# Performance work log

Hardware: AMD Instinct MI355X
Metric: run time of the kernel (lower is better)

Reference implementation:

```python
import jax, jax.numpy as jnp
import numpy as np

D = 1024      # in_dim
HS = 64       # head_size
H = 16        # num_heads
B, S = 2, 2048


def setup_inputs() -> dict:
    key = jax.random.key(0)
    k1, k2, k3, k4, k5, k6 = jax.random.split(key, 6)
    scale = 1.0 / np.sqrt(D)
    x = jax.random.normal(k1, (B, S, D), dtype=jnp.float32)
    # Stacked per-head projection weights (torch Linear weight is [out,in];
    # random init so layout only needs to be consistent). query weight exists
    # in the torch module but is never used (source bug), so it is omitted.
    Wk = jax.random.normal(k2, (H, D, HS), dtype=jnp.float32) * scale
    Wv = jax.random.normal(k3, (H, D, HS), dtype=jnp.float32) * scale
    Wproj = jax.random.normal(k4, (H * HS, D), dtype=jnp.float32) * (1.0 / np.sqrt(H * HS))
    bproj = jax.random.normal(k5, (D,), dtype=jnp.float32) * 0.01
    return {"x": x, "Wk": Wk, "Wv": Wv, "Wproj": Wproj, "bproj": bproj}


def reference(x, Wk, Wv, Wproj, bproj):
    # Faithful to source: k = key(x); q = value(x); v = value(x)  (q == v, no softmax)
    k = jnp.einsum("bsd,hde->bhse", x, Wk)   # [B,H,S,HS]
    v = jnp.einsum("bsd,hde->bhse", x, Wv)   # [B,H,S,HS]
    q = v
    inv_sqrt = jnp.asarray(HS, x.dtype) ** -0.5
    wei = jnp.einsum("bhse,bhte->bhst", q, k) * inv_sqrt  # [B,H,S,S], unnormalized
    out = jnp.einsum("bhst,bhte->bhse", wei, v)            # [B,H,S,HS]
    # concat heads: [B,S,H*HS]
    out = jnp.transpose(out, (0, 2, 1, 3)).reshape(x.shape[0], x.shape[1], H * HS)
    return out @ Wproj + bproj  # [B,S,D]
```

## Files before the change

kernel.cpp:

```cpp
#include <hip/hip_runtime.h>

#define B_ 2
#define S_ 2048
#define D_ 1024
#define H_ 16
#define HS_ 64
#define HD_ 1024
#define BS_ (B_*S_)
#define KS_ 64
#define TP_ 136

typedef __attribute__((ext_vector_type(8))) short short8_t;
typedef __attribute__((ext_vector_type(4))) float float4_t;

__device__ inline unsigned short f32_to_bf16(float f) {
  unsigned int u = __float_as_uint(f);
  u += 0x7FFF + ((u >> 16) & 1);
  return (unsigned short)(u >> 16);
}

__device__ inline void async_copy16(const void* g, void* lds) {
  __builtin_amdgcn_global_load_lds(
      (const __attribute__((address_space(1))) void*)g,
      (__attribute__((address_space(3))) void*)lds, 16, 0, 0);
}


__global__ __launch_bounds__(256) void prep_kernel(
    const float* __restrict__ x, const float* __restrict__ Wk,
    const float* __restrict__ Wv, unsigned short* __restrict__ xb,
    unsigned short* __restrict__ Wkvt) {
  const int blk = blockIdx.x;
  const int tid = threadIdx.x;
  __shared__ float lds[64][65];
  if (blk < 4096) {
    int idx = blk * 256 + tid;
    float4 v = ((const float4*)x)[idx];
    ushort4 o;
    o.x = f32_to_bf16(v.x); o.y = f32_to_bf16(v.y);
    o.z = f32_to_bf16(v.z); o.w = f32_to_bf16(v.w);
    ((ushort4*)xb)[idx] = o;
    return;
  }
  const int wblk = blk - 4096;
  const int h = wblk >> 4;
  const int d0 = (wblk & 15) * 64;
#pragma unroll
  for (int i = 0; i < 16; ++i) {
    int idx = tid + i * 256; int dd = idx >> 6, e = idx & 63;
    lds[e][dd] = Wk[((size_t)h * D_ + d0 + dd) * HS_ + e];
  }
  __syncthreads();
#pragma unroll
  for (int i = 0; i < 16; ++i) {
    int idx = tid + i * 256; int e = idx >> 6, dd = idx & 63;
    Wkvt[((size_t)h * 128 + e) * D_ + d0 + dd] = f32_to_bf16(lds[e][dd]);
  }
  __syncthreads();
#pragma unroll
  for (int i = 0; i < 16; ++i) {
    int idx = tid + i * 256; int dd = idx >> 6, e = idx & 63;
    lds[e][dd] = Wv[((size_t)h * D_ + d0 + dd) * HS_ + e];
  }
  __syncthreads();
#pragma unroll
  for (int i = 0; i < 16; ++i) {
    int idx = tid + i * 256; int e = idx >> 6, dd = idx & 63;
    Wkvt[((size_t)h * 128 + 64 + e) * D_ + d0 + dd] = f32_to_bf16(lds[e][dd]);
  }
}

__global__ __launch_bounds__(256) void kv_mfma_kernel(
    const unsigned short* __restrict__ xb,
    const unsigned short* __restrict__ Wkvt,
    unsigned short* __restrict__ Vb,
    float* __restrict__ Mpart) {
  const int blk = blockIdx.x;
  const int stile = blk & 31;
  const int h = blk >> 5;
  const int s0 = stile * 128;
  const int tid = threadIdx.x;
  const int lane = tid & 63;
  const int wid = tid >> 6;
  const int wm = wid & 1, wn = wid >> 1;
  const int quad = lane >> 4, l16 = lane & 15;
  const int srow8 = lane >> 3;
  const int sc8 = lane & 7;
  const int xa = l16 & 7;

  __shared__ __align__(16) unsigned char smem[65536];
  unsigned short* const A0 = (unsigned short*)smem;
  unsigned short* const B0 = (unsigned short*)(smem + 16384);
  unsigned short* const A1 = (unsigned short*)(smem + 32768);
  unsigned short* const B1 = (unsigned short*)(smem + 49152);
  unsigned short* Ktl = (unsigned short*)smem;
  unsigned short* Vtl = (unsigned short*)(smem + 64 * TP_ * 2);

  float4_t acc[4][4];
  const float4_t fz = {0.f, 0.f, 0.f, 0.f};
#pragma unroll
  for (int i = 0; i < 4; ++i)
#pragma unroll
    for (int j = 0; j < 4; ++j) acc[i][j] = fz;

  auto stage = [&](int kt, unsigned short* Ad, unsigned short* Bd) {
    const int k0 = kt * KS_;
#pragma unroll
    for (int i = 0; i < 4; ++i) {
      int g = wid * 4 + i;
      int r = g * 8 + srow8;
      int ch = (sc8 ^ (r & 7)) * 8;
      async_copy16(xb + (size_t)(s0 + r) * D_ + k0 + ch, Ad + g * 8 * KS_);
      async_copy16(Wkvt + ((size_t)h * 128 + r) * D_ + k0 + ch, Bd + g * 8 * KS_);
    }
  };
  auto compute = [&](const unsigned short* Ac, const unsigned short* Bc) {
#pragma unroll
    for (int ks = 0; ks < 2; ++ks) {
      short8_t a[4], b[4];
#pragma unroll
      for (int mi = 0; mi < 4; ++mi)
        a[mi] = *(const short8_t*)(Ac + (wm * 64 + mi * 16 + l16) * KS_ +
                                   ((ks * 4 + quad) ^ xa) * 8);
#pragma unroll
      for (int ni = 0; ni < 4; ++ni)
        b[ni] = *(const short8_t*)(Bc + (wn * 64 + ni * 16 + l16) * KS_ +
                                   ((ks * 4 + quad) ^ xa) * 8);
      __builtin_amdgcn_s_setprio(1);
#pragma unroll
      for (int mi = 0; mi < 4; ++mi)
#pragma unroll
        for (int ni = 0; ni < 4; ++ni)
          acc[mi][ni] = __builtin_amdgcn_mfma_f32_16x16x32_bf16(
              a[mi], b[ni], acc[mi][ni], 0, 0, 0);
      __builtin_amdgcn_s_setprio(0);
    }
  };

  stage(0, A0, B0);
#pragma unroll
  for (int t = 0; t < 16; ++t) {
    unsigned short* Ac = (t & 1) ? A1 : A0;
    unsigned short* Bc = (t & 1) ? B1 : B0;
    if (t < 15) {
      stage(t + 1, (t & 1) ? A0 : A1, (t & 1) ? B0 : B1);
      asm volatile("s_waitcnt vmcnt(8)" ::: "memory");
    } else {
      asm volatile("s_waitcnt vmcnt(0)" ::: "memory");
    }
    __builtin_amdgcn_s_barrier();
    __builtin_amdgcn_sched_barrier(0);
    compute(Ac, Bc);
    __builtin_amdgcn_sched_barrier(0);
    __builtin_amdgcn_s_barrier();
  }

  {
    unsigned short* dstT = (wn == 0) ? Ktl : Vtl;
#pragma unroll
    for (int mi = 0; mi < 4; ++mi)
#pragma unroll
      for (int ni = 0; ni < 4; ++ni) {
        int f = ni * 16 + l16;
        int sm = wm * 64 + mi * 16 + quad * 4;
        ushort4 o;
        o.x = f32_to_bf16(acc[mi][ni][0]);
        o.y = f32_to_bf16(acc[mi][ni][1]);
        o.z = f32_to_bf16(acc[mi][ni][2]);
        o.w = f32_to_bf16(acc[mi][ni][3]);
        *(ushort4*)&dstT[f * TP_ + sm] = o;
      }
  }
  __syncthreads();

#pragma unroll
  for (int u = 0; u < 4; ++u) {
    int unit = tid + u * 256;
    int s = unit & 127;
    int ec = (unit >> 7) * 8;
    union { unsigned short u16[8]; uint4 v; } t;
#pragma unroll
    for (int e = 0; e < 8; ++e) t.u16[e] = Vtl[(ec + e) * TP_ + s];
    *(uint4*)&Vb[(size_t)(s0 + s) * HD_ + h * 64 + ec] = t.v;
  }

  {
    float4_t macc[4];
#pragma unroll
    for (int ni = 0; ni < 4; ++ni) macc[ni] = fz;
#pragma unroll
    for (int ss = 0; ss < 4; ++ss) {
      short8_t ka = *(const short8_t*)&Ktl[(wid * 16 + l16) * TP_ + ss * 32 + quad * 8];
#pragma unroll
      for (int ni = 0; ni < 4; ++ni) {
        short8_t vv = *(const short8_t*)&Vtl[(ni * 16 + l16) * TP_ + ss * 32 + quad * 8];
        macc[ni] = __builtin_amdgcn_mfma_f32_16x16x32_bf16(ka, vv, macc[ni], 0, 0, 0);
      }
    }
    float* mdst = Mpart + ((size_t)stile * H_ + h) * 4096;
#pragma unroll
    for (int ni = 0; ni < 4; ++ni) {
      int e = ni * 16 + l16;
#pragma unroll
      for (int r = 0; r < 4; ++r) {
        int f = wid * 16 + quad * 4 + r;
        mdst[f * 64 + e] = macc[ni][r];
      }
    }
  }
}

__global__ __launch_bounds__(256) void m_reduce_kernel(
    const float* __restrict__ Mpart, float* __restrict__ M) {
  const int gid = blockIdx.x * 256 + threadIdx.x;
  const int e0 = gid * 4;
  const int bh = e0 >> 12;
  const int idx = e0 & 4095;
  const int b = bh >> 4, h = bh & 15;
  float4 s = {0.f, 0.f, 0.f, 0.f};
#pragma unroll
  for (int p = 0; p < 16; ++p) {
    const float4 v =
        *(const float4*)&Mpart[(((size_t)(b * 16 + p)) * H_ + h) * 4096 + idx];
    s.x += v.x; s.y += v.y; s.z += v.z; s.w += v.w;
  }
  s.x *= 0.125f; s.y *= 0.125f; s.z *= 0.125f; s.w *= 0.125f;
  *(float4*)&M[(size_t)bh * 4096 + idx] = s;
}

__global__ __launch_bounds__(256) void p_kernel(
    const float* __restrict__ M, const float* __restrict__ Wproj,
    unsigned short* __restrict__ Pt) {
  const int blk = blockIdx.x;
  const int dtile = blk & 15;
  const int h = (blk >> 4) & 15;
  const int b = blk >> 8;
  const int d0 = dtile * 64;
  const int tid = threadIdx.x;
  const int tx = tid & 15, ty = tid >> 4;
  __shared__ float Ms[64][68];
  __shared__ float Ws[64][68];
  const size_t mbase = ((size_t)(b * H_ + h)) * HS_ * HS_;
#pragma unroll
  for (int i = 0; i < 16; ++i) {
    int idx = tid + i * 256;
    int f = idx >> 6, e = idx & 63;
    Ms[e][f] = M[mbase + idx];
    Ws[f][e] = Wproj[(size_t)(h * HS_ + f) * D_ + d0 + e];
  }
  __syncthreads();
  float acc[4][4] = {};
#pragma unroll
  for (int kk = 0; kk < 64; ++kk) {
    const float4 a4 = *(const float4*)&Ms[kk][ty * 4];
    const float4 b4 = *(const float4*)&Ws[kk][tx * 4];
    const float a[4] = {a4.x, a4.y, a4.z, a4.w};
    const float bb[4] = {b4.x, b4.y, b4.z, b4.w};
#pragma unroll
    for (int i = 0; i < 4; ++i)
#pragma unroll
      for (int j = 0; j < 4; ++j) acc[i][j] += a[i] * bb[j];
  }
  __syncthreads();
#pragma unroll
  for (int i = 0; i < 4; ++i)
#pragma unroll
    for (int j = 0; j < 4; ++j)
      Ms[tx * 4 + j][ty * 4 + i] = acc[i][j];
  __syncthreads();
  {
    int c = tid >> 2, ch = tid & 3;
    unsigned short* dst = Pt + ((size_t)(b * D_ + d0 + c)) * HD_ + h * 64 + ch * 16;
#pragma unroll
    for (int e = 0; e < 16; ++e) dst[e] = f32_to_bf16(Ms[c][ch * 16 + e]);
  }
}

__global__ __launch_bounds__(256) void out_mfma_kernel(
    const unsigned short* __restrict__ Vb,
    const unsigned short* __restrict__ Pt,
    const float* __restrict__ bproj,
    float* __restrict__ out) {
  const int blk = blockIdx.x;
  const int ntile = blk & 15;
  const int stile = blk >> 4;
  const int s0 = stile * 128;
  const int n0 = ntile * 64;
  const int b = s0 >> 11;
  const int tid = threadIdx.x;
  const int lane = tid & 63;
  const int wid = tid >> 6;
  const int wm = wid & 1, wn = wid >> 1;
  const int quad = lane >> 4, l16 = lane & 15;
  const int srow8 = lane >> 3;
  const int sc8 = lane & 7;
  const int xa = l16 & 7;

  __shared__ __align__(16) unsigned char smem[49152];
  unsigned short* const A0 = (unsigned short*)smem;
  unsigned short* const B0 = (unsigned short*)(smem + 16384);
  unsigned short* const A1 = (unsigned short*)(smem + 24576);
  unsigned short* const B1 = (unsigned short*)(smem + 40960);

  float4_t acc[4][2];
  const float4_t fz = {0.f, 0.f, 0.f, 0.f};
#pragma unroll
  for (int i = 0; i < 4; ++i)
#pragma unroll
    for (int j = 0; j < 2; ++j) acc[i][j] = fz;

  const unsigned short* Bpanel = Pt + (size_t)b * D_ * HD_;
  auto stage = [&](int kt, unsigned short* Ad, unsigned short* Bd) {
    const int k0 = kt * KS_;
#pragma unroll
    for (int i = 0; i < 4; ++i) {
      int g = wid * 4 + i;
      int r = g * 8 + srow8;
      int ch = (sc8 ^ (r & 7)) * 8;
      async_copy16(Vb + (size_t)(s0 + r) * HD_ + k0 + ch, Ad + g * 8 * KS_);
    }
#pragma unroll
    for (int i = 0; i < 2; ++i) {
      int g = wid * 2 + i;
      int r = g * 8 + srow8;
      int ch = (sc8 ^ (r & 7)) * 8;
      async_copy16(Bpanel + (size_t)(n0 + r) * HD_ + k0 + ch, Bd + g * 8 * KS_);
    }
  };
  auto compute = [&](const unsigned short* Ac, const unsigned short* Bc) {
#pragma unroll
    for (int ks = 0; ks < 2; ++ks) {
      short8_t a[4], bfr[2];
#pragma unroll
      for (int mi = 0; mi < 4; ++mi)
        a[mi] = *(const short8_t*)(Ac + (wm * 64 + mi * 16 + l16) * KS_ +
                                   ((ks * 4 + quad) ^ xa) * 8);
#pragma unroll
      for (int ni = 0; ni < 2; ++ni)
        bfr[ni] = *(const short8_t*)(Bc + (wn * 32 + ni * 16 + l16) * KS_ +
                                     ((ks * 4 + quad) ^ xa) * 8);
      __builtin_amdgcn_s_setprio(1);
#pragma unroll
      for (int mi = 0; mi < 4; ++mi)
#pragma unroll
        for (int ni = 0; ni < 2; ++ni)
          acc[mi][ni] = __builtin_amdgcn_mfma_f32_16x16x32_bf16(
              a[mi], bfr[ni], acc[mi][ni], 0, 0, 0);
      __builtin_amdgcn_s_setprio(0);
    }
  };

  stage(0, A0, B0);
#pragma unroll
  for (int t = 0; t < 16; ++t) {
    unsigned short* Ac = (t & 1) ? A1 : A0;
    unsigned short* Bc = (t & 1) ? B1 : B0;
    if (t < 15) {
      stage(t + 1, (t & 1) ? A0 : A1, (t & 1) ? B0 : B1);
      asm volatile("s_waitcnt vmcnt(6)" ::: "memory");
    } else {
      asm volatile("s_waitcnt vmcnt(0)" ::: "memory");
    }
    __builtin_amdgcn_s_barrier();
    __builtin_amdgcn_sched_barrier(0);
    compute(Ac, Bc);
    __builtin_amdgcn_sched_barrier(0);
    __builtin_amdgcn_s_barrier();
  }

#pragma unroll
  for (int ni = 0; ni < 2; ++ni) {
    int col = n0 + wn * 32 + ni * 16 + l16;
    float bias = bproj[col];
#pragma unroll
    for (int mi = 0; mi < 4; ++mi) {
      int rowb = s0 + wm * 64 + mi * 16 + quad * 4;
#pragma unroll
      for (int r = 0; r < 4; ++r)
        out[(size_t)(rowb + r) * D_ + col] = acc[mi][ni][r] + bias;
    }
  }
}

extern "C" void kernel_launch(void* const* d_in, const int* in_sizes, int n_in,
                              void* d_out, int out_size, void* d_ws, size_t ws_size,
                              hipStream_t stream) {
  const float* x = (const float*)d_in[0];
  const float* Wk = (const float*)d_in[1];
  const float* Wv = (const float*)d_in[2];
  const float* Wproj = (const float*)d_in[3];
  const float* bproj = (const float*)d_in[4];
  float* out = (float*)d_out;

  char* ws = (char*)d_ws;
  unsigned short* xb = (unsigned short*)ws;
  unsigned short* Wkvt = xb + (size_t)BS_ * D_;
  unsigned short* Vb = Wkvt + (size_t)H_ * 128 * D_;
  float* Mpart = (float*)(Vb + (size_t)BS_ * HD_);
  float* M = Mpart + (size_t)32 * H_ * 4096;
  unsigned short* Pt = (unsigned short*)(M + (size_t)B_ * H_ * 4096);

  prep_kernel<<<dim3(4096 + H_ * (D_ / 64)), dim3(256), 0, stream>>>(x, Wk, Wv, xb, Wkvt);
  kv_mfma_kernel<<<dim3(32 * H_), dim3(256), 0, stream>>>(xb, Wkvt, Vb, Mpart);
  m_reduce_kernel<<<dim3(128), dim3(256), 0, stream>>>(Mpart, M);
  p_kernel<<<dim3(B_ * H_ * (D_ / 64)), dim3(256), 0, stream>>>(M, Wproj, Pt);
  out_mfma_kernel<<<dim3(32 * 16), dim3(256), 0, stream>>>(Vb, Pt, bproj, out);
}
```

Baseline: 128.4 us.

## Double block tiles to 512 threads and split K-step loads into two phases

The KV projection kernel now covers 256 sequence rows per block with 8 waves, and the output GEMM covers 128 columns per block, so each weight/P tile loaded into LDS is reused across more rows. Each K-step's staging is split in two halves, with the second half issued between the two MFMA sub-phases so loads are spread across the compute. The M partial products are still written per 128-row half, so the reduce layout is unchanged. This trades fewer blocks (256 vs 512) and larger LDS footprint for better reuse, at the risk of lower occupancy and extra barriers per iteration.

```diff
diff --git a/kernel.cpp b/kernel.cpp
--- a/kernel.cpp
+++ b/kernel.cpp
@@ -8,7 +8,7 @@
 #define HD_ 1024
 #define BS_ (B_*S_)
 #define KS_ 64
-#define TP_ 136
+#define TP2_ 264
 
 typedef __attribute__((ext_vector_type(8))) short short8_t;
 typedef __attribute__((ext_vector_type(4))) float float4_t;
@@ -70,31 +70,31 @@
   }
 }
 
-__global__ __launch_bounds__(256) void kv_mfma_kernel(
+__global__ __launch_bounds__(512) void kv_mfma_kernel(
     const unsigned short* __restrict__ xb,
     const unsigned short* __restrict__ Wkvt,
     unsigned short* __restrict__ Vb,
     float* __restrict__ Mpart) {
   const int blk = blockIdx.x;
-  const int stile = blk & 31;
-  const int h = blk >> 5;
-  const int s0 = stile * 128;
+  const int stile = blk & 15;
+  const int h = blk >> 4;
+  const int s0 = stile * 256;
   const int tid = threadIdx.x;
   const int lane = tid & 63;
   const int wid = tid >> 6;
-  const int wm = wid & 1, wn = wid >> 1;
+  const int wm = wid >> 1, wn = wid & 1;
   const int quad = lane >> 4, l16 = lane & 15;
   const int srow8 = lane >> 3;
   const int sc8 = lane & 7;
   const int xa = l16 & 7;
 
-  __shared__ __align__(16) unsigned char smem[65536];
+  __shared__ __align__(16) unsigned char smem[98304];
   unsigned short* const A0 = (unsigned short*)smem;
-  unsigned short* const B0 = (unsigned short*)(smem + 16384);
-  unsigned short* const A1 = (unsigned short*)(smem + 32768);
-  unsigned short* const B1 = (unsigned short*)(smem + 49152);
-  unsigned short* Ktl = (unsigned short*)smem;
-  unsigned short* Vtl = (unsigned short*)(smem + 64 * TP_ * 2);
+  unsigned short* const B0 = (unsigned short*)(smem + 32768);
+  unsigned short* const A1 = (unsigned short*)(smem + 49152);
+  unsigned short* const B1 = (unsigned short*)(smem + 81920);
+  unsigned short* const Ktl = (unsigned short*)smem;
+  unsigned short* const Vtl = (unsigned short*)(smem + 64 * TP2_ * 2);
 
   float4_t acc[4][4];
   const float4_t fz = {0.f, 0.f, 0.f, 0.f};
@@ -103,54 +103,65 @@
 #pragma unroll
     for (int j = 0; j < 4; ++j) acc[i][j] = fz;
 
-  auto stage = [&](int kt, unsigned short* Ad, unsigned short* Bd) {
+  auto stage_half = [&](int kt, unsigned short* Ad, unsigned short* Bd, int hf) {
     const int k0 = kt * KS_;
 #pragma unroll
-    for (int i = 0; i < 4; ++i) {
-      int g = wid * 4 + i;
+    for (int i = 0; i < 2; ++i) {
+      int g = wid * 4 + hf * 2 + i;
       int r = g * 8 + srow8;
       int ch = (sc8 ^ (r & 7)) * 8;
       async_copy16(xb + (size_t)(s0 + r) * D_ + k0 + ch, Ad + g * 8 * KS_);
+    }
+    {
+      int g = wid * 2 + hf;
+      int r = g * 8 + srow8;
+      int ch = (sc8 ^ (r & 7)) * 8;
       async_copy16(Wkvt + ((size_t)h * 128 + r) * D_ + k0 + ch, Bd + g * 8 * KS_);
     }
   };
-  auto compute = [&](const unsigned short* Ac, const unsigned short* Bc) {
-#pragma unroll
-    for (int ks = 0; ks < 2; ++ks) {
-      short8_t a[4], b[4];
-#pragma unroll
-      for (int mi = 0; mi < 4; ++mi)
-        a[mi] = *(const short8_t*)(Ac + (wm * 64 + mi * 16 + l16) * KS_ +
-                                   ((ks * 4 + quad) ^ xa) * 8);
+  auto compute_phase = [&](const unsigned short* Ac, const unsigned short* Bc,
+                           int ks) {
+    short8_t a[4], b[4];
+#pragma unroll
+    for (int mi = 0; mi < 4; ++mi)
+      a[mi] = *(const short8_t*)(Ac + (wm * 64 + mi * 16 + l16) * KS_ +
+                                 ((ks * 4 + quad) ^ xa) * 8);
+#pragma unroll
+    for (int ni = 0; ni < 4; ++ni)
+      b[ni] = *(const short8_t*)(Bc + (wn * 64 + ni * 16 + l16) * KS_ +
+                                 ((ks * 4 + quad) ^ xa) * 8);
+    __builtin_amdgcn_s_setprio(1);
+#pragma unroll
+    for (int mi = 0; mi < 4; ++mi)
 #pragma unroll
       for (int ni = 0; ni < 4; ++ni)
-        b[ni] = *(const short8_t*)(Bc + (wn * 64 + ni * 16 + l16) * KS_ +
-                                   ((ks * 4 + quad) ^ xa) * 8);
-      __builtin_amdgcn_s_setprio(1);
-#pragma unroll
-      for (int mi = 0; mi < 4; ++mi)
-#pragma unroll
-        for (int ni = 0; ni < 4; ++ni)
-          acc[mi][ni] = __builtin_amdgcn_mfma_f32_16x16x32_bf16(
-              a[mi], b[ni], acc[mi][ni], 0, 0, 0);
-      __builtin_amdgcn_s_setprio(0);
-    }
+        acc[mi][ni] = __builtin_amdgcn_mfma_f32_16x16x32_bf16(
+            a[mi], b[ni], acc[mi][ni], 0, 0, 0);
+    __builtin_amdgcn_s_setprio(0);
   };
 
-  stage(0, A0, B0);
-#pragma unroll
+  stage_half(0, A0, B0, 0);
+  stage_half(0, A0, B0, 1);
   for (int t = 0; t < 16; ++t) {
     unsigned short* Ac = (t & 1) ? A1 : A0;
     unsigned short* Bc = (t & 1) ? B1 : B0;
+    unsigned short* An = (t & 1) ? A0 : A1;
+    unsigned short* Bn = (t & 1) ? B0 : B1;
     if (t < 15) {
-      stage(t + 1, (t & 1) ? A0 : A1, (t & 1) ? B0 : B1);
-      asm volatile("s_waitcnt vmcnt(8)" ::: "memory");
+      stage_half(t + 1, An, Bn, 0);
+      asm volatile("s_waitcnt vmcnt(3)" ::: "memory");
     } else {
       asm volatile("s_waitcnt vmcnt(0)" ::: "memory");
     }
     __builtin_amdgcn_s_barrier();
     __builtin_amdgcn_sched_barrier(0);
-    compute(Ac, Bc);
+    compute_phase(Ac, Bc, 0);
+    __builtin_amdgcn_sched_barrier(0);
+    __builtin_amdgcn_s_barrier();
+    if (t < 15) stage_half(t + 1, An, Bn, 1);
+    __builtin_amdgcn_s_barrier();
+    __builtin_amdgcn_sched_barrier(0);
+    compute_phase(Ac, Bc, 1);
     __builtin_amdgcn_sched_barrier(0);
     __builtin_amdgcn_s_barrier();
   }
@@ -168,42 +179,45 @@
         o.y = f32_to_bf16(acc[mi][ni][1]);
         o.z = f32_to_bf16(acc[mi][ni][2]);
         o.w = f32_to_bf16(acc[mi][ni][3]);
-        *(ushort4*)&dstT[f * TP_ + sm] = o;
+        *(ushort4*)&dstT[f * TP2_ + sm] = o;
       }
   }
   __syncthreads();
 
 #pragma unroll
   for (int u = 0; u < 4; ++u) {
-    int unit = tid + u * 256;
-    int s = unit & 127;
-    int ec = (unit >> 7) * 8;
-    union { unsigned short u16[8]; uint4 v; } t;
-#pragma unroll
-    for (int e = 0; e < 8; ++e) t.u16[e] = Vtl[(ec + e) * TP_ + s];
-    *(uint4*)&Vb[(size_t)(s0 + s) * HD_ + h * 64 + ec] = t.v;
+    int unit = tid + u * 512;
+    int s = unit & 255;
+    int ec = (unit >> 8) * 8;
+    union { unsigned short u16[8]; uint4 v; } tv;
+#pragma unroll
+    for (int e = 0; e < 8; ++e) tv.u16[e] = Vtl[(ec + e) * TP2_ + s];
+    *(uint4*)&Vb[(size_t)(s0 + s) * HD_ + h * 64 + ec] = tv.v;
   }
 
   {
+    const int half = wid >> 2, fq = wid & 3;
     float4_t macc[4];
 #pragma unroll
     for (int ni = 0; ni < 4; ++ni) macc[ni] = fz;
 #pragma unroll
     for (int ss = 0; ss < 4; ++ss) {
-      short8_t ka = *(const short8_t*)&Ktl[(wid * 16 + l16) * TP_ + ss * 32 + quad * 8];
+      short8_t ka = *(const short8_t*)&Ktl[(fq * 16 + l16) * TP2_ +
+                                           half * 128 + ss * 32 + quad * 8];
 #pragma unroll
       for (int ni = 0; ni < 4; ++ni) {
-        short8_t vv = *(const short8_t*)&Vtl[(ni * 16 + l16) * TP_ + ss * 32 + quad * 8];
+        short8_t vv = *(const short8_t*)&Vtl[(ni * 16 + l16) * TP2_ +
+                                             half * 128 + ss * 32 + quad * 8];
         macc[ni] = __builtin_amdgcn_mfma_f32_16x16x32_bf16(ka, vv, macc[ni], 0, 0, 0);
       }
     }
-    float* mdst = Mpart + ((size_t)stile * H_ + h) * 4096;
+    float* mdst = Mpart + (((size_t)(stile * 2 + half)) * H_ + h) * 4096;
 #pragma unroll
     for (int ni = 0; ni < 4; ++ni) {
       int e = ni * 16 + l16;
 #pragma unroll
       for (int r = 0; r < 4; ++r) {
-        int f = wid * 16 + quad * 4 + r;
+        int f = fq * 16 + quad * 4 + r;
         mdst[f * 64 + e] = macc[ni][r];
       }
     }
@@ -276,16 +290,16 @@
   }
 }
 
-__global__ __launch_bounds__(256) void out_mfma_kernel(
+__global__ __launch_bounds__(512) void out_mfma_kernel(
     const unsigned short* __restrict__ Vb,
     const unsigned short* __restrict__ Pt,
     const float* __restrict__ bproj,
     float* __restrict__ out) {
   const int blk = blockIdx.x;
-  const int ntile = blk & 15;
-  const int stile = blk >> 4;
+  const int ntile = blk & 7;
+  const int stile = blk >> 3;
   const int s0 = stile * 128;
-  const int n0 = ntile * 64;
+  const int n0 = ntile * 128;
   const int b = s0 >> 11;
   const int tid = threadIdx.x;
   const int lane = tid & 63;
@@ -296,11 +310,11 @@
   const int sc8 = lane & 7;
   const int xa = l16 & 7;
 
-  __shared__ __align__(16) unsigned char smem[49152];
+  __shared__ __align__(16) unsigned char smem[65536];
   unsigned short* const A0 = (unsigned short*)smem;
   unsigned short* const B0 = (unsigned short*)(smem + 16384);
-  unsigned short* const A1 = (unsigned short*)(smem + 24576);
-  unsigned short* const B1 = (unsigned short*)(smem + 40960);
+  unsigned short* const A1 = (unsigned short*)(smem + 32768);
+  unsigned short* const B1 = (unsigned short*)(smem + 49152);
 
   float4_t acc[4][2];
   const float4_t fz = {0.f, 0.f, 0.f, 0.f};
@@ -310,60 +324,64 @@
     for (int j = 0; j < 2; ++j) acc[i][j] = fz;
 
   const unsigned short* Bpanel = Pt + (size_t)b * D_ * HD_;
-  auto stage = [&](int kt, unsigned short* Ad, unsigned short* Bd) {
+  auto stage_half = [&](int kt, unsigned short* Ad, unsigned short* Bd, int hf) {
     const int k0 = kt * KS_;
-#pragma unroll
-    for (int i = 0; i < 4; ++i) {
-      int g = wid * 4 + i;
+    {
+      int g = wid * 2 + hf;
       int r = g * 8 + srow8;
       int ch = (sc8 ^ (r & 7)) * 8;
       async_copy16(Vb + (size_t)(s0 + r) * HD_ + k0 + ch, Ad + g * 8 * KS_);
     }
-#pragma unroll
-    for (int i = 0; i < 2; ++i) {
-      int g = wid * 2 + i;
+    {
+      int g = wid * 2 + hf;
       int r = g * 8 + srow8;
       int ch = (sc8 ^ (r & 7)) * 8;
       async_copy16(Bpanel + (size_t)(n0 + r) * HD_ + k0 + ch, Bd + g * 8 * KS_);
     }
   };
-  auto compute = [&](const unsigned short* Ac, const unsigned short* Bc) {
-#pragma unroll
-    for (int ks = 0; ks < 2; ++ks) {
-      short8_t a[4], bfr[2];
-#pragma unroll
-      for (int mi = 0; mi < 4; ++mi)
-        a[mi] = *(const short8_t*)(Ac + (wm * 64 + mi * 16 + l16) * KS_ +
+  auto compute_phase = [&](const unsigned short* Ac, const unsigned short* Bc,
+                           int ks) {
+    short8_t a[4], bfr[2];
+#pragma unroll
+    for (int mi = 0; mi < 4; ++mi)
+      a[mi] = *(const short8_t*)(Ac + (wm * 64 + mi * 16 + l16) * KS_ +
+                                 ((ks * 4 + quad) ^ xa) * 8);
+#pragma unroll
+    for (int ni = 0; ni < 2; ++ni)
+      bfr[ni] = *(const short8_t*)(Bc + (wn * 32 + ni * 16 + l16) * KS_ +
                                    ((ks * 4 + quad) ^ xa) * 8);
+    __builtin_amdgcn_s_setprio(1);
+#pragma unroll
+    for (int mi = 0; mi < 4; ++mi)
 #pragma unroll
       for (int ni = 0; ni < 2; ++ni)
-        bfr[ni] = *(const short8_t*)(Bc + (wn * 32 + ni * 16 + l16) * KS_ +
-                                     ((ks * 4 + quad) ^ xa) * 8);
-      __builtin_amdgcn_s_setprio(1);
-#pragma unroll
-      for (int mi = 0; mi < 4; ++mi)
-#pragma unroll
-        for (int ni = 0; ni < 2; ++ni)
-          acc[mi][ni] = __builtin_amdgcn_mfma_f32_16x16x32_bf16(
-              a[mi], bfr[ni], acc[mi][ni], 0, 0, 0);
-      __builtin_amdgcn_s_setprio(0);
-    }
+        acc[mi][ni] = __builtin_amdgcn_mfma_f32_16x16x32_bf16(
+            a[mi], bfr[ni], acc[mi][ni], 0, 0, 0);
+    __builtin_amdgcn_s_setprio(0);
   };
 
-  stage(0, A0, B0);
-#pragma unroll
+  stage_half(0, A0, B0, 0);
+  stage_half(0, A0, B0, 1);
   for (int t = 0; t < 16; ++t) {
     unsigned short* Ac = (t & 1) ? A1 : A0;
     unsigned short* Bc = (t & 1) ? B1 : B0;
+    unsigned short* An = (t & 1) ? A0 : A1;
+    unsigned short* Bn = (t & 1) ? B0 : B1;
     if (t < 15) {
-      stage(t + 1, (t & 1) ? A0 : A1, (t & 1) ? B0 : B1);
-      asm volatile("s_waitcnt vmcnt(6)" ::: "memory");
+      stage_half(t + 1, An, Bn, 0);
+      asm volatile("s_waitcnt vmcnt(2)" ::: "memory");
     } else {
       asm volatile("s_waitcnt vmcnt(0)" ::: "memory");
     }
     __builtin_amdgcn_s_barrier();
     __builtin_amdgcn_sched_barrier(0);
-    compute(Ac, Bc);
+    compute_phase(Ac, Bc, 0);
+    __builtin_amdgcn_sched_barrier(0);
+    __builtin_amdgcn_s_barrier();
+    if (t < 15) stage_half(t + 1, An, Bn, 1);
+    __builtin_amdgcn_s_barrier();
+    __builtin_amdgcn_sched_barrier(0);
+    compute_phase(Ac, Bc, 1);
     __builtin_amdgcn_sched_barrier(0);
     __builtin_amdgcn_s_barrier();
   }
@@ -401,8 +419,8 @@
   unsigned short* Pt = (unsigned short*)(M + (size_t)B_ * H_ * 4096);
 
   prep_kernel<<<dim3(4096 + H_ * (D_ / 64)), dim3(256), 0, stream>>>(x, Wk, Wv, xb, Wkvt);
-  kv_mfma_kernel<<<dim3(32 * H_), dim3(256), 0, stream>>>(xb, Wkvt, Vb, Mpart);
+  kv_mfma_kernel<<<dim3(16 * H_), dim3(512), 0, stream>>>(xb, Wkvt, Vb, Mpart);
   m_reduce_kernel<<<dim3(128), dim3(256), 0, stream>>>(Mpart, M);
   p_kernel<<<dim3(B_ * H_ * (D_ / 64)), dim3(256), 0, stream>>>(M, Wproj, Pt);
-  out_mfma_kernel<<<dim3(32 * 16), dim3(256), 0, stream>>>(Vb, Pt, bproj, out);
-}
+  out_mfma_kernel<<<dim3(32 * 8), dim3(512), 0, stream>>>(Vb, Pt, bproj, out);
+}
```

Result: no change. 130.7 us (+1.8%).
